# Optimization experiments

Measured on AMD Instinct MI355X. Metric: run time of the kernel, lower is better.

## Reference

```python
import jax, jax.numpy as jnp
import numpy as np

BS = 64; T = 96; C = 16; IN = 16; H = 256; NH = 8; DH = H // NH
NCLS = 4; L = T + NCLS; LAYERS = 4; GDEP = 2; EPS = 1e-5


def _ln(x, g, b):
    m = x.mean(-1, keepdims=True)
    v = ((x - m) ** 2).mean(-1, keepdims=True)
    return (x - m) / jnp.sqrt(v + EPS) * g + b


def _mask():
    # causal upper-triangular -inf mask; last NCLS rows (cls tokens) attend everywhere
    m = jnp.where(jnp.triu(jnp.ones((L, L), jnp.float32), 1) > 0, -jnp.inf, 0.0)
    return m.at[-NCLS:].set(0.0)


def _enc(h, mask, Wqkv, bqkv, Wo, bo, W1, b1, W2, b2, g1, be1, g2, be2):
    # post-norm TransformerEncoderLayer (torch default), dropout=0
    B = h.shape[0]
    qkv = h @ Wqkv.T + bqkv
    q, k, v = jnp.split(qkv, 3, axis=-1)
    sp = lambda t: t.reshape(B, L, NH, DH).transpose(0, 2, 1, 3)
    q, k, v = sp(q), sp(k), sp(v)
    s = jnp.einsum('bhqd,bhkd->bhqk', q, k) / np.float32(np.sqrt(DH)) + mask
    a = jax.nn.softmax(s, axis=-1)
    o = jnp.einsum('bhqk,bhkd->bhqd', a, v).transpose(0, 2, 1, 3).reshape(B, L, H)
    h = _ln(h + o @ Wo.T + bo, g1, be1)
    ff = jax.nn.relu(h @ W1.T + b1) @ W2.T + b2
    return _ln(h + ff, g2, be2)


def _mixprop(x, g, Wm, bm):
    # x: (bs, H, C, NCLS); MTGNN mixprop with alpha=0
    adj = g + jnp.eye(C, dtype=g.dtype)
    a = adj / adj.sum(1, keepdims=True)
    h = x
    outs = [x]
    for _ in range(GDEP):
        h = jnp.einsum('ncwl,vw->ncvl', h, a)
        outs.append(h)
    ho = jnp.concatenate(outs, axis=1)  # (bs, (GDEP+1)*H, C, NCLS)
    return jnp.einsum('ncwl,oc->nowl', ho, Wm) + bm[None, :, None, None]


def _forward(x, Wfc, bfc, cls_token, pos_emb, emb1, emb2, Wl1, bl1, Wl2, bl2,
             Wqkv, bqkv, Wo, bo, W1, b1, W2, b2, ln1g, ln1b, ln2g, ln2b,
             Wmlp, bmlp, Wd1, bd1, Wd2, bd2):
    bs = x.shape[0]
    h = x @ Wfc.T + bfc                                      # (bs,T,C,H)
    h = jnp.concatenate([h, jnp.broadcast_to(cls_token, (bs, NCLS, C, H))], axis=1)
    h = h + pos_emb[None]                                    # (bs,L,C,H)
    h = jnp.swapaxes(h, 1, 2).reshape(bs * C, L, H)
    mask = _mask()
    # graph_constructor (alpha=1)
    m1 = jnp.tanh(emb1 @ Wl1.T + bl1)
    m2 = jnp.tanh(emb2 @ Wl2.T + bl2)
    g = jax.nn.relu(jnp.tanh(m1 @ m2.T - m2 @ m1.T))         # (C,C)
    h = _enc(h, mask, Wqkv[0], bqkv[0], Wo[0], bo[0], W1[0], b1[0], W2[0], b2[0],
             ln1g[0], ln1b[0], ln2g[0], ln2b[0])
    for l in range(1, LAYERS):
        cls = h[:, -NCLS:].reshape(bs, C, NCLS, H).transpose(0, 3, 1, 2)  # (bs,H,C,NCLS)
        cls = _mixprop(cls, g, Wmlp[l - 1], bmlp[l - 1])
        cls = cls.transpose(0, 2, 3, 1).reshape(bs * C, NCLS, H)
        h = jnp.concatenate([h[:, :-NCLS], cls], axis=1)
        h = _enc(h, mask, Wqkv[l], bqkv[l], Wo[l], bo[l], W1[l], b1[l], W2[l], b2[l],
                 ln1g[l], ln1b[l], ln2g[l], ln2b[l])
    z = jnp.tanh(h[:, -NCLS:].reshape(bs, C * NCLS * H))
    z = jax.nn.gelu(z @ Wd1.T + bd1, approximate=False) @ Wd2.T + bd2
    return z[:, 0]


def setup_inputs() -> dict:
    key = jax.random.key(0)
    ks = iter(jax.random.split(key, 64))
    rn = lambda *s: jax.random.normal(next(ks), s, dtype=jnp.float32) * 0.05
    d = {}
    d['x'] = jax.random.normal(next(ks), (BS, T, C, IN), dtype=jnp.float32)
    d['p'] = jnp.zeros((BS,), jnp.float32)
    d['y'] = jnp.zeros((BS,), jnp.float32)
    d['Wfc'] = rn(H, IN); d['bfc'] = jnp.zeros((H,), jnp.float32)
    d['cls_token'] = rn(1, NCLS, C, H) * 20.0  # torch randn scale ~1
    d['pos_emb'] = rn(NCLS + T, C, H) * 20.0
    d['emb1'] = rn(C, H); d['emb2'] = rn(C, H)
    d['Wl1'] = rn(H, H); d['bl1'] = jnp.zeros((H,), jnp.float32)
    d['Wl2'] = rn(H, H); d['bl2'] = jnp.zeros((H,), jnp.float32)
    d['Wqkv'] = rn(LAYERS, 3 * H, H); d['bqkv'] = jnp.zeros((LAYERS, 3 * H), jnp.float32)
    d['Wo'] = rn(LAYERS, H, H); d['bo'] = jnp.zeros((LAYERS, H), jnp.float32)
    d['W1'] = rn(LAYERS, 4 * H, H); d['b1'] = jnp.zeros((LAYERS, 4 * H), jnp.float32)
    d['W2'] = rn(LAYERS, H, 4 * H); d['b2'] = jnp.zeros((LAYERS, H), jnp.float32)
    d['ln1g'] = jnp.ones((LAYERS, H), jnp.float32); d['ln1b'] = jnp.zeros((LAYERS, H), jnp.float32)
    d['ln2g'] = jnp.ones((LAYERS, H), jnp.float32); d['ln2b'] = jnp.zeros((LAYERS, H), jnp.float32)
    d['Wmlp'] = rn(LAYERS - 1, H, (GDEP + 1) * H); d['bmlp'] = jnp.zeros((LAYERS - 1, H), jnp.float32)
    d['Wd1'] = rn(H, NCLS * C * H); d['bd1'] = jnp.zeros((H,), jnp.float32)
    d['Wd2'] = rn(1, H); d['bd2'] = jnp.zeros((1,), jnp.float32)
    return d


def reference(x, p, y, Wfc, bfc, cls_token, pos_emb, emb1, emb2, Wl1, bl1, Wl2, bl2,
              Wqkv, bqkv, Wo, bo, W1, b1, W2, b2, ln1g, ln1b, ln2g, ln2b,
              Wmlp, bmlp, Wd1, bd1, Wd2, bd2):
    # p, y are unused by the original forward (kept for signature parity)
    return _forward(x, Wfc, bfc, cls_token, pos_emb, emb1, emb2, Wl1, bl1, Wl2, bl2,
                    Wqkv, bqkv, Wo, bo, W1, b1, W2, b2, ln1g, ln1b, ln2g, ln2b,
                    Wmlp, bmlp, Wd1, bd1, Wd2, bd2)
```

## Files before the change

kernel.cpp:

```cpp
#include <hip/hip_runtime.h>
#include <hip/hip_bf16.h>
#include <math.h>

typedef unsigned short u16;
typedef unsigned int   u32;
typedef __attribute__((ext_vector_type(8))) short short8;
typedef __attribute__((ext_vector_type(4))) float f32x4;

#define BSZ   64
#define TT    96
#define CCH   16
#define INDIM 16
#define HD    256
#define NHEAD 8
#define DHEAD 32
#define NCLS  4
#define LSEQ  100
#define NLAY  4
#define EPSV  1e-5f
#define BSEQ  (BSZ*CCH)
#define MTOK  (BSEQ*LSEQ)

#if __has_builtin(__builtin_amdgcn_exp2f)
#define EXP2F __builtin_amdgcn_exp2f
#else
#define EXP2F exp2f
#endif

__device__ __forceinline__ float bf2f(u16 x){ return __uint_as_float(((u32)x)<<16); }
__device__ __forceinline__ u16 f2bf(float f){
    u32 u = __float_as_uint(f);
    u32 r = (u + 0x7fffu + ((u>>16)&1u)) >> 16;
    return (u16)r;
}
__device__ __forceinline__ float lo16(u32 r){ return __uint_as_float(r<<16); }
__device__ __forceinline__ float hi16(u32 r){ return __uint_as_float(r&0xffff0000u); }

__device__ __forceinline__ u32 cvtpk(float lo, float hi){
    u32 r;
    asm("v_cvt_pk_bf16_f32 %0, %1, %2" : "=v"(r) : "v"(lo), "v"(hi));
    return r;
}

__device__ __forceinline__ void gload_lds16(const u16* g, u16* l){
    __builtin_amdgcn_global_load_lds(
        (const __attribute__((address_space(1))) unsigned int*)g,
        (__attribute__((address_space(3))) unsigned int*)l, 16, 0, 0);
}

__global__ __launch_bounds__(256)
void k_cvt(const float* __restrict__ src, u16* __restrict__ dst, int n)
{
    for (int i = blockIdx.x*256 + threadIdx.x; i < n; i += gridDim.x*256)
        dst[i] = f2bf(src[i]);
}

__global__ __launch_bounds__(256)
void k_embed(const float* __restrict__ x, const float* __restrict__ Wfc,
             const float* __restrict__ bfc, const float* __restrict__ cls,
             const float* __restrict__ pos, u16* __restrict__ h)
{
    int s = blockIdx.x;
    int n = s >> 4, c = s & 15;
    int hc = threadIdx.x;
    float wr[INDIM];
    #pragma unroll
    for (int i=0;i<INDIM;i++) wr[i] = Wfc[hc*INDIM + i];
    float bb = bfc[hc];
    for (int l=0; l<TT; l++){
        const float* xr = x + (size_t)((n*TT + l)*CCH + c)*INDIM;
        float acc = bb;
        #pragma unroll
        for (int i=0;i<INDIM;i++) acc += xr[i]*wr[i];
        acc += pos[(size_t)(l*CCH + c)*HD + hc];
        h[((size_t)s*LSEQ + l)*HD + hc] = f2bf(acc);
    }
    #pragma unroll
    for (int l=TT; l<LSEQ; l++){
        float v = cls[(size_t)((l-TT)*CCH + c)*HD + hc]
                + pos[(size_t)(l*CCH + c)*HD + hc];
        h[((size_t)s*LSEQ + l)*HD + hc] = f2bf(v);
    }
}

__global__ __launch_bounds__(256)
void k_graph_m(const float* __restrict__ emb, const float* __restrict__ Wl,
               const float* __restrict__ bl, float* __restrict__ m)
{
    int r = blockIdx.x, o = threadIdx.x;
    __shared__ float e[HD];
    e[o] = emb[r*HD + o];
    __syncthreads();
    const float* w = Wl + (size_t)o*HD;
    float acc = bl[o];
    for (int k=0;k<HD;k++) acc += e[k]*w[k];
    m[r*HD + o] = tanhf(acc);
}

__global__ __launch_bounds__(256)
void k_graph_a(const float* __restrict__ m1, const float* __restrict__ m2,
               float* __restrict__ a)
{
    int t = threadIdx.x; int v = t >> 4, w = t & 15;
    __shared__ float adj[16][17];
    float s1=0.f, s2=0.f;
    for (int k=0;k<HD;k++){
        s1 += m1[v*HD+k]*m2[w*HD+k];
        s2 += m2[v*HD+k]*m1[w*HD+k];
    }
    float g = tanhf(s1 - s2); g = g > 0.f ? g : 0.f;
    adj[v][w] = g + (v==w ? 1.f : 0.f);
    __syncthreads();
    float rs = 0.f;
    #pragma unroll
    for (int j=0;j<16;j++) rs += adj[v][j];
    a[t] = adj[v][w] / rs;
}

__global__ __launch_bounds__(256)
void k_gemmA(const u16* __restrict__ A, int lda,
             const u16* __restrict__ W, const float* __restrict__ bias,
             u16* __restrict__ C, int ldc, int K, int relu, int scat)
{
    __shared__ u16 smem[32768];
    u16* As0 = smem;
    u16* As1 = smem + 8192;
    u16* Ws0 = smem + 16384;
    u16* Ws1 = smem + 24576;

    int t = threadIdx.x;
    int lane = t & 63, w = t >> 6;
    int wm = (w & 1)*64, wn = (w >> 1)*64;
    int fr = lane & 15, quad = lane >> 4;

    int nwg = gridDim.x * gridDim.y;
    int bid = blockIdx.y * gridDim.x + blockIdx.x;
    int tile = bid;
    if (!(nwg & 7)){
        int cpx = nwg >> 3;
        tile = (bid & 7)*cpx + (bid >> 3);
    }
    int bx = tile % gridDim.x, by = tile / gridDim.x;
    size_t mb = (size_t)by * 128;
    int nb = bx * 128;

    int srow = lane >> 2;
    int sslot = lane & 3;

    f32x4 acc[4][4] = {};

    auto STAGE = [&](int bb, int k0){
        #pragma unroll
        for (int i=0;i<2;i++){
            int r = w*32 + i*16 + srow;
            int cw = sslot ^ ((r>>1)&3);
            gload_lds16(&A[(mb + r)*(size_t)lda + k0      + cw*8], &As0[bb*4096 + (w*32 + i*16)*32]);
            gload_lds16(&A[(mb + r)*(size_t)lda + k0 + 32 + cw*8], &As1[bb*4096 + (w*32 + i*16)*32]);
            gload_lds16(&W[(size_t)(nb + r)*K   + k0      + cw*8], &Ws0[bb*4096 + (w*32 + i*16)*32]);
            gload_lds16(&W[(size_t)(nb + r)*K   + k0 + 32 + cw*8], &Ws1[bb*4096 + (w*32 + i*16)*32]);
        }
    };
    auto COMPUTE = [&](int bb){
        short8 af0[4], af1[4], bf0[4], bf1[4];
        #pragma unroll
        for (int mt=0; mt<4; mt++){
            int r = wm + mt*16 + fr;
            int sw = (quad ^ ((r>>1)&3)) << 3;
            af0[mt] = *(const short8*)&As0[bb*4096 + r*32 + sw];
            af1[mt] = *(const short8*)&As1[bb*4096 + r*32 + sw];
        }
        #pragma unroll
        for (int nt=0; nt<4; nt++){
            int r = wn + nt*16 + fr;
            int sw = (quad ^ ((r>>1)&3)) << 3;
            bf0[nt] = *(const short8*)&Ws0[bb*4096 + r*32 + sw];
            bf1[nt] = *(const short8*)&Ws1[bb*4096 + r*32 + sw];
        }
        #pragma unroll
        for (int mt=0; mt<4; mt++)
            #pragma unroll
            for (int nt=0; nt<4; nt++){
                acc[mt][nt] = __builtin_amdgcn_mfma_f32_16x16x32_bf16(
                    af0[mt], bf0[nt], acc[mt][nt], 0, 0, 0);
                acc[mt][nt] = __builtin_amdgcn_mfma_f32_16x16x32_bf16(
                    af1[mt], bf1[nt], acc[mt][nt], 0, 0, 0);
            }
    };

    const int nst = K >> 6;
    STAGE(0, 0);
    asm volatile("s_waitcnt vmcnt(0)" ::: "memory");
    __builtin_amdgcn_s_barrier();
    int b = 0;
    for (int ts = 0; ts < nst; ++ts){
        if (ts + 1 < nst) STAGE(b^1, (ts+1) << 6);
        COMPUTE(b);
        asm volatile("s_waitcnt vmcnt(0)" ::: "memory");
        __builtin_amdgcn_s_barrier();
        b ^= 1;
    }

    float bb4[4];
    #pragma unroll
    for (int nt=0; nt<4; nt++) bb4[nt] = bias[nb + wn + nt*16 + fr];
    __syncthreads();
    u16* Ct = smem;
    #pragma unroll
    for (int mt=0; mt<4; mt++){
        int rw = wm + mt*16 + quad*4;
        #pragma unroll
        for (int nt=0; nt<4; nt++){
            int col = wn + nt*16 + fr;
            float v0 = acc[mt][nt][0] + bb4[nt];
            float v1 = acc[mt][nt][1] + bb4[nt];
            float v2 = acc[mt][nt][2] + bb4[nt];
            float v3 = acc[mt][nt][3] + bb4[nt];
            if (relu){
                v0 = v0 > 0.f ? v0 : 0.f;  v1 = v1 > 0.f ? v1 : 0.f;
                v2 = v2 > 0.f ? v2 : 0.f;  v3 = v3 > 0.f ? v3 : 0.f;
            }
            u32 p01 = cvtpk(v0, v1), p23 = cvtpk(v2, v3);
            Ct[(rw+0)*128 + col] = (u16)p01;
            Ct[(rw+1)*128 + col] = (u16)(p01 >> 16);
            Ct[(rw+2)*128 + col] = (u16)p23;
            Ct[(rw+3)*128 + col] = (u16)(p23 >> 16);
        }
    }
    __syncthreads();
    #pragma unroll
    for (int it=0; it<8; ++it){
        int row = it*16 + (t>>4);
        int seg = t & 15;
        size_t rg = mb + row;
        if (scat) rg = (rg >> 2)*LSEQ + TT + (rg & 3);
        *(short8*)&C[rg*(size_t)ldc + nb + seg*8] = *(const short8*)&Ct[row*128 + seg*8];
    }
}

__global__ __launch_bounds__(256)
void k_gemmC(const u16* __restrict__ A, int lda, int K,
             const u16* __restrict__ W, const float* __restrict__ bias,
             u16* __restrict__ h, const float* __restrict__ gam,
             const float* __restrict__ bet, size_t row0)
{
    __shared__ u16 smem[40960];
    u16* As0 = smem;
    u16* As1 = smem + 4096;
    u16* Ws0 = smem + 8192;
    u16* Ws1 = smem + 24576;

    int t = threadIdx.x;
    int lane = t & 63, w = t >> 6;
    int fr = lane & 15, quad = lane >> 4;
    size_t mb = (size_t)blockIdx.x * 64;
    int srow = lane >> 2, sslot = lane & 3;

    f32x4 acc[4][4] = {};

    auto STAGE = [&](int bb, int k0){
        {
            int r = w*16 + srow;
            int cw = sslot ^ ((r>>1)&3);
            gload_lds16(&A[(mb + r)*(size_t)lda + k0      + cw*8], &As0[bb*2048 + (w*16)*32]);
            gload_lds16(&A[(mb + r)*(size_t)lda + k0 + 32 + cw*8], &As1[bb*2048 + (w*16)*32]);
        }
        #pragma unroll
        for (int i=0;i<4;i++){
            int r = w*64 + i*16 + srow;
            int cw = sslot ^ ((r>>1)&3);
            gload_lds16(&W[(size_t)r*K + k0      + cw*8], &Ws0[bb*8192 + (w*64 + i*16)*32]);
            gload_lds16(&W[(size_t)r*K + k0 + 32 + cw*8], &Ws1[bb*8192 + (w*64 + i*16)*32]);
        }
    };
    auto COMPUTE = [&](int bb){
        short8 af0[4], af1[4], bf0[4], bf1[4];
        #pragma unroll
        for (int mt=0; mt<4; mt++){
            int ra = mt*16 + fr;
            int swa = (quad ^ ((ra>>1)&3)) << 3;
            af0[mt] = *(const short8*)&As0[bb*2048 + ra*32 + swa];
            af1[mt] = *(const short8*)&As1[bb*2048 + ra*32 + swa];
        }
        #pragma unroll
        for (int nt=0; nt<4; nt++){
            int rb = w*64 + nt*16 + fr;
            int swb = (quad ^ ((rb>>1)&3)) << 3;
            bf0[nt] = *(const short8*)&Ws0[bb*8192 + rb*32 + swb];
            bf1[nt] = *(const short8*)&Ws1[bb*8192 + rb*32 + swb];
        }
        #pragma unroll
        for (int mt=0; mt<4; mt++)
            #pragma unroll
            for (int nt=0; nt<4; nt++){
                acc[mt][nt] = __builtin_amdgcn_mfma_f32_16x16x32_bf16(
                    af0[mt], bf0[nt], acc[mt][nt], 0, 0, 0);
                acc[mt][nt] = __builtin_amdgcn_mfma_f32_16x16x32_bf16(
                    af1[mt], bf1[nt], acc[mt][nt], 0, 0, 0);
            }
    };

    const int nst = K >> 6;
    STAGE(0, 0);
    asm volatile("s_waitcnt vmcnt(0)" ::: "memory");
    __builtin_amdgcn_s_barrier();
    int b = 0;
    for (int ts = 0; ts < nst; ++ts){
        if (ts + 1 < nst) STAGE(b^1, (ts+1) << 6);
        COMPUTE(b);
        asm volatile("s_waitcnt vmcnt(0)" ::: "memory");
        __builtin_amdgcn_s_barrier();
        b ^= 1;
    }

    float bb4[4], gg[4], be[4];
    #pragma unroll
    for (int nt=0; nt<4; nt++){
        int col = w*64 + nt*16 + fr;
        bb4[nt] = bias[col]; gg[nt] = gam[col]; be[nt] = bet[col];
    }
    #pragma unroll
    for (int mt=0; mt<4; mt++){
        #pragma unroll
        for (int r=0; r<4; r++){
            size_t row = row0 + mb + mt*16 + quad*4 + r;
            #pragma unroll
            for (int nt=0; nt<4; nt++)
                acc[mt][nt][r] += bb4[nt] + bf2f(h[row*HD + w*64 + nt*16 + fr]);
        }
    }
    __syncthreads();
    float* red  = (float*)smem;
    float* red2 = (float*)(smem + 512);
    float ps[4][4];
    #pragma unroll
    for (int mt=0; mt<4; mt++)
        #pragma unroll
        for (int r=0; r<4; r++){
            float s = acc[mt][0][r] + acc[mt][1][r] + acc[mt][2][r] + acc[mt][3][r];
            s += __shfl_xor(s,1,64); s += __shfl_xor(s,2,64);
            s += __shfl_xor(s,4,64); s += __shfl_xor(s,8,64);
            ps[mt][r] = s;
        }
    if (fr == 0){
        #pragma unroll
        for (int mt=0; mt<4; mt++)
            #pragma unroll
            for (int r=0; r<4; r++)
                red[w*64 + mt*16 + quad*4 + r] = ps[mt][r];
    }
    __syncthreads();
    float mean[4][4];
    #pragma unroll
    for (int mt=0; mt<4; mt++)
        #pragma unroll
        for (int r=0; r<4; r++){
            int rl = mt*16 + quad*4 + r;
            mean[mt][r] = (red[rl] + red[64+rl] + red[128+rl] + red[192+rl]) * (1.f/256.f);
            float s = 0.f;
            #pragma unroll
            for (int nt=0; nt<4; nt++){ float d = acc[mt][nt][r] - mean[mt][r]; s += d*d; }
            s += __shfl_xor(s,1,64); s += __shfl_xor(s,2,64);
            s += __shfl_xor(s,4,64); s += __shfl_xor(s,8,64);
            ps[mt][r] = s;
        }
    if (fr == 0){
        #pragma unroll
        for (int mt=0; mt<4; mt++)
            #pragma unroll
            for (int r=0; r<4; r++)
                red2[w*64 + mt*16 + quad*4 + r] = ps[mt][r];
    }
    __syncthreads();
    u16* Ct = smem + 8192;
    #pragma unroll
    for (int mt=0; mt<4; mt++)
        #pragma unroll
        for (int r=0; r<4; r++){
            int rl = mt*16 + quad*4 + r;
            float inv = rsqrtf((red2[rl] + red2[64+rl] + red2[128+rl] + red2[192+rl])
                               * (1.f/256.f) + EPSV);
            float o0 = (acc[mt][0][r] - mean[mt][r]) * inv * gg[0] + be[0];
            float o1 = (acc[mt][1][r] - mean[mt][r]) * inv * gg[1] + be[1];
            float o2 = (acc[mt][2][r] - mean[mt][r]) * inv * gg[2] + be[2];
            float o3 = (acc[mt][3][r] - mean[mt][r]) * inv * gg[3] + be[3];
            u32 p01 = cvtpk(o0, o1), p23 = cvtpk(o2, o3);
            Ct[rl*256 + w*64 +  0 + fr] = (u16)p01;
            Ct[rl*256 + w*64 + 16 + fr] = (u16)(p01 >> 16);
            Ct[rl*256 + w*64 + 32 + fr] = (u16)p23;
            Ct[rl*256 + w*64 + 48 + fr] = (u16)(p23 >> 16);
        }
    __syncthreads();
    #pragma unroll
    for (int it=0; it<8; ++it){
        int row = it*8 + (t>>5);
        int seg = t & 31;
        *(short8*)&h[(row0 + mb + row)*HD + seg*8] = *(const short8*)&Ct[row*256 + seg*8];
    }
}

#define KS_STR 40
#define VT_STR 136
__global__ __launch_bounds__(256)
void k_attn(u16* __restrict__ qkv)
{
    __shared__ u16 smem[17664];
    int t = threadIdx.x;
    int w = t >> 6, lane = t & 63;
    int fr = lane & 15, quad = lane >> 4;
    int p = t >> 7, t2 = t & 127;
    u16* Ks = smem + p*4480;
    u16* Vt = smem + 8960 + p*4352;

    {
        int gp = blockIdx.x*2 + p;
        size_t base = (size_t)(gp >> 3)*LSEQ*768 + (gp & 7)*32;
        for (int idx = t2; idx < 1792; idx += 128){
            int key = idx >> 4, d2 = (idx & 15) << 1;
            u32 kv = (key < LSEQ) ? *(const u32*)&qkv[base + (size_t)key*768 + 256 + d2] : 0u;
            *(u32*)&Ks[key*KS_STR + d2] = kv;
        }
        for (int idx = t2; idx < 2048; idx += 128){
            int key = idx & 127, d2 = (idx >> 7) << 1;
            u32 vv = (key < LSEQ) ? *(const u32*)&qkv[base + (size_t)key*768 + 512 + d2] : 0u;
            Vt[ d2   *VT_STR + key] = (u16)(vv & 0xffffu);
            Vt[(d2+1)*VT_STR + key] = (u16)(vv >> 16);
        }
    }
    __syncthreads();

    int wp = w >> 1;
    int gp = blockIdx.x*2 + wp;
    size_t base = (size_t)(gp >> 3)*LSEQ*768 + (gp & 7)*32;
    u16* Ksw = smem + wp*4480;
    u16* Vtw = smem + 8960 + wp*4352;

    short8 kf[7];
    #pragma unroll
    for (int nt=0; nt<7; nt++)
        kf[nt] = *(const short8*)&Ksw[(nt*16 + fr)*KS_STR + quad*8];
    short8 vfr[4][2];
    #pragma unroll
    for (int ks=0; ks<4; ks++)
        #pragma unroll
        for (int nt=0; nt<2; nt++)
            vfr[ks][nt] = *(const short8*)&Vtw[(nt*16 + fr)*VT_STR + ks*32 + quad*8];

    const int smask = (w & 1) ? 0x34 : 0x4B;
    short8 qfs[7];
    #pragma unroll
    for (int st=0; st<7; ++st){
        if (!((smask >> st) & 1)) continue;
        int q = st*16 + fr;
        short8 z = {};
        qfs[st] = (q < LSEQ) ? *(const short8*)&qkv[base + (size_t)q*768 + quad*8] : z;
    }
    __syncthreads();

    u16* Ph = smem + w*2048;
    u16* Pv = smem + 8960 + w*2048;

    const float cs = 0.17677669529663687f * 1.4426950408889634f;
    #pragma unroll
    for (int st = 0; st < 7; ++st){
        if (!((smask >> st) & 1)) continue;
        const int ntile = (st == 6) ? 7 : (st + 1);
        const int nks   = (st == 6) ? 4 : (st/2 + 1);
        f32x4 S[7];
        #pragma unroll
        for (int nt=0; nt<7; nt++){
            if (nt >= ntile) continue;
            f32x4 z = {};
            S[nt] = __builtin_amdgcn_mfma_f32_16x16x32_bf16(qfs[st], kf[nt], z, 0,0,0);
        }
        float mx[4] = {-1e30f,-1e30f,-1e30f,-1e30f};
        #pragma unroll
        for (int nt=0;nt<7;nt++){
            if (nt >= ntile) continue;
            #pragma unroll
            for (int r=0;r<4;r++){
                float s = S[nt][r]*cs;
                if (nt == ntile-1){
                    int qr = st*16 + quad*4 + r;
                    int jmax = (qr < TT) ? qr : (LSEQ-1);
                    s = ((nt*16 + fr) <= jmax) ? s : -1e30f;
                }
                S[nt][r] = s;
                mx[r] = fmaxf(mx[r], s);
            }
        }
        #pragma unroll
        for (int r=0;r<4;r++){
            #pragma unroll
            for (int m=1;m<16;m<<=1) mx[r] = fmaxf(mx[r], __shfl_xor(mx[r], m, 64));
        }
        float l4[4] = {0.f,0.f,0.f,0.f};
        #pragma unroll
        for (int r=0;r<4;r++){
            #pragma unroll
            for (int nt=0;nt<7;nt++){
                if (nt >= ntile) continue;
                float pv = EXP2F(S[nt][r] - mx[r]);
                S[nt][r] = pv;
                l4[r] += pv;
            }
        }
        #pragma unroll
        for (int r=0;r<4;r++){
            #pragma unroll
            for (int m=1;m<16;m<<=1) l4[r] += __shfl_xor(l4[r], m, 64);
        }
        asm volatile("s_waitcnt lgkmcnt(0)" ::: "memory");
        #pragma unroll
        for (int nt=0;nt<7;nt++){
            if (nt >= ntile) continue;
            u32 h01 = cvtpk(S[nt][0], S[nt][1]);
            u32 h23 = cvtpk(S[nt][2], S[nt][3]);
            float l0 = S[nt][0] - lo16(h01);
            float l1 = S[nt][1] - hi16(h01);
            float l2 = S[nt][2] - lo16(h23);
            float l3 = S[nt][3] - hi16(h23);
            u32 g01 = cvtpk(l0, l1);
            u32 g23 = cvtpk(l2, l3);
            u16 hv[4] = {(u16)h01, (u16)(h01>>16), (u16)h23, (u16)(h23>>16)};
            u16 lv[4] = {(u16)g01, (u16)(g01>>16), (u16)g23, (u16)(g23>>16)};
            #pragma unroll
            for (int r=0;r<4;r++){
                int row = quad*4 + r;
                int a = (nt>>1)*512 + row*32 + ((((nt&1)<<4) + fr) ^ (((row>>1)&3)<<3));
                Ph[a] = hv[r];
                Pv[a] = lv[r];
            }
        }
        if (ntile*16 < nks*32){
            #pragma unroll
            for (int r=0;r<4;r++){
                int row = quad*4 + r;
                int a = (ntile>>1)*512 + row*32 + ((((ntile&1)<<4) + fr) ^ (((row>>1)&3)<<3));
                Ph[a] = 0;
                Pv[a] = 0;
            }
        }
        asm volatile("s_waitcnt lgkmcnt(0)" ::: "memory");
        f32x4 D[2] = {};
        #pragma unroll
        for (int ks=0; ks<4; ks++){
            if (ks >= nks) continue;
            int a = ks*512 + fr*32 + ((quad ^ ((fr>>1)&3)) << 3);
            short8 ph = *(const short8*)&Ph[a];
            short8 pl = *(const short8*)&Pv[a];
            #pragma unroll
            for (int nt=0; nt<2; nt++){
                D[nt] = __builtin_amdgcn_mfma_f32_16x16x32_bf16(ph, vfr[ks][nt], D[nt], 0,0,0);
                D[nt] = __builtin_amdgcn_mfma_f32_16x16x32_bf16(pl, vfr[ks][nt], D[nt], 0,0,0);
            }
        }
        #pragma unroll
        for (int r=0;r<4;r++){
            int qr = st*16 + quad*4 + r;
            if (qr < LSEQ){
                float inv = 1.f / l4[r];
                u32 o = cvtpk(D[0][r]*inv, D[1][r]*inv);
                qkv[base + (size_t)qr*768 +      fr] = (u16)o;
                qkv[base + (size_t)qr*768 + 16 + fr] = (u16)(o >> 16);
            }
        }
    }
}

__global__ __launch_bounds__(256)
void k_mixprep(const u16* __restrict__ h, const float* __restrict__ a,
               u16* __restrict__ amid)
{
    int n = blockIdx.x >> 2, tt = blockIdx.x & 3;
    __shared__ float xs[256][17], h1s[256][17], h2s[256][17];
    __shared__ float as[16][17];
    int t = threadIdx.x;
    as[t>>4][t&15] = a[t];
    for (int idx=t; idx<4096; idx+=256){
        int w = idx >> 8, hc = idx & 255;
        xs[hc][w] = bf2f(h[((size_t)(n*16 + w)*LSEQ + TT + tt)*HD + hc]);
    }
    __syncthreads();
    for (int idx=t; idx<4096; idx+=256){
        int v = idx & 15, hc = idx >> 4;
        float acc = 0.f;
        #pragma unroll
        for (int w=0;w<16;w++) acc += as[v][w]*xs[hc][w];
        h1s[hc][v] = acc;
    }
    __syncthreads();
    for (int idx=t; idx<4096; idx+=256){
        int v = idx & 15, hc = idx >> 4;
        float acc = 0.f;
        #pragma unroll
        for (int w=0;w<16;w++) acc += as[v][w]*h1s[hc][w];
        h2s[hc][v] = acc;
    }
    __syncthreads();
    int hc = t;
    #pragma unroll
    for (int w=0;w<16;w++){
        size_t row = (size_t)((n*16 + w)*4 + tt);
        amid[row*768 +       hc] = f2bf(xs[hc][w]);
        amid[row*768 + 256 + hc] = f2bf(h1s[hc][w]);
        amid[row*768 + 512 + hc] = f2bf(h2s[hc][w]);
    }
}

__global__ __launch_bounds__(256)
void k_z(const u16* __restrict__ h, u16* __restrict__ z)
{
    int bid = blockIdx.x, t = threadIdx.x;
    #pragma unroll
    for (int tc=0;tc<4;tc++)
        z[((size_t)bid*4 + tc)*HD + t] = f2bf(tanhf(bf2f(h[((size_t)bid*LSEQ + TT + tc)*HD + t])));
}

__global__ __launch_bounds__(256)
void k_head1p(const u16* __restrict__ z, const float* __restrict__ Wd1,
              float* __restrict__ d1p)
{
    __shared__ float zch[64][137];
    __shared__ float wt[16][137];
    int t = threadIdx.x;
    int col = t & 15, rgrp = t >> 4;
    int ob = blockIdx.x * 16;
    int kb = blockIdx.y;
    float acc[4] = {0.f,0.f,0.f,0.f};
    for (int kc=0; kc<1024; kc+=128){
        int base_k = kb*1024 + kc;
        #pragma unroll
        for (int jj=0; jj<16; jj++){
            int idx = t + jj*256;
            int n = idx >> 6, k2 = (idx & 63) << 1;
            u32 r = *(const u32*)&z[(size_t)n*16384 + base_k + k2];
            zch[n][k2] = lo16(r); zch[n][k2+1] = hi16(r);
        }
        #pragma unroll
        for (int jj=0; jj<2; jj++){
            int idx = t + jj*256;
            int r = idx >> 5, k4 = (idx & 31) << 2;
            float4 w4 = *(const float4*)&Wd1[(size_t)(ob + r)*16384 + base_k + k4];
            wt[r][k4] = w4.x; wt[r][k4+1] = w4.y; wt[r][k4+2] = w4.z; wt[r][k4+3] = w4.w;
        }
        __syncthreads();
        for (int k=0;k<128;k++){
            float wv = wt[col][k];
            #pragma unroll
            for (int u=0;u<4;u++) acc[u] += zch[rgrp + 16*u][k]*wv;
        }
        __syncthreads();
    }
    #pragma unroll
    for (int u=0;u<4;u++)
        d1p[(size_t)(kb*64 + rgrp + 16*u)*HD + ob + col] = acc[u];
}

__global__ __launch_bounds__(256)
void k_headf(const float* __restrict__ d1p, const float* __restrict__ bd1,
             const float* __restrict__ Wd2, const float* __restrict__ bd2,
             float* __restrict__ out)
{
    __shared__ float red[4];
    int n = blockIdx.x, c = threadIdx.x;
    float s = 0.f;
    #pragma unroll
    for (int kb=0; kb<16; kb++) s += d1p[(size_t)(kb*64 + n)*HD + c];
    float xx = s + bd1[c];
    float ge = 0.5f*xx*(1.f + erff(xx*0.70710678118654752f));
    float p = ge * Wd2[c];
    #pragma unroll
    for (int m=1;m<64;m<<=1) p += __shfl_xor(p, m, 64);
    if ((c & 63) == 0) red[c >> 6] = p;
    __syncthreads();
    if (c == 0) out[n] = red[0]+red[1]+red[2]+red[3] + bd2[0];
}

extern "C" void kernel_launch(void* const* d_in, const int* in_sizes, int n_in,
                              void* d_out, int out_size, void* d_ws, size_t ws_size,
                              hipStream_t stream)
{
    const float* x    = (const float*)d_in[0];
    const float* Wfc  = (const float*)d_in[3];
    const float* bfc  = (const float*)d_in[4];
    const float* cls  = (const float*)d_in[5];
    const float* pos  = (const float*)d_in[6];
    const float* emb1 = (const float*)d_in[7];
    const float* emb2 = (const float*)d_in[8];
    const float* Wl1  = (const float*)d_in[9];
    const float* bl1  = (const float*)d_in[10];
    const float* Wl2  = (const float*)d_in[11];
    const float* bl2  = (const float*)d_in[12];
    const float* Wqkv = (const float*)d_in[13];
    const float* bqkv = (const float*)d_in[14];
    const float* Wo   = (const float*)d_in[15];
    const float* bo   = (const float*)d_in[16];
    const float* W1   = (const float*)d_in[17];
    const float* b1   = (const float*)d_in[18];
    const float* W2   = (const float*)d_in[19];
    const float* b2   = (const float*)d_in[20];
    const float* ln1g = (const float*)d_in[21];
    const float* ln1b = (const float*)d_in[22];
    const float* ln2g = (const float*)d_in[23];
    const float* ln2b = (const float*)d_in[24];
    const float* Wmlp = (const float*)d_in[25];
    const float* bmlp = (const float*)d_in[26];
    const float* Wd1  = (const float*)d_in[27];
    const float* bd1  = (const float*)d_in[28];
    const float* Wd2  = (const float*)d_in[29];
    const float* bd2  = (const float*)d_in[30];

    int NCH = 8;
    {
        const size_t fixed = 63145088 + (1<<20);
        if      (fixed + (size_t)MTOK    *2048 <= ws_size) NCH = 1;
        else if (fixed + (size_t)(MTOK/2)*2048 <= ws_size) NCH = 2;
        else if (fixed + (size_t)(MTOK/4)*2048 <= ws_size) NCH = 4;
    }
    const int RCH = MTOK / NCH;
    const int SCH = BSEQ / NCH;

    u16* h    = (u16*)d_ws;
    u16* buf  = h    + (size_t)MTOK*HD;
    u16* wq   = buf  + (size_t)RCH*1024;
    u16* wo   = wq   + (size_t)4*768*256;
    u16* w1   = wo   + (size_t)4*256*256;
    u16* w2   = w1   + (size_t)4*1024*256;
    u16* wmb  = w2   + (size_t)4*256*1024;
    u16* zb   = wmb  + (size_t)3*256*768;
    float* fp = (float*)(zb + (size_t)BSZ*16384);
    float* m1  = fp;
    float* m2  = m1 + CCH*HD;
    float* an  = m2 + CCH*HD;
    float* d1p = an + CCH*CCH;

    k_cvt<<<512, 256, 0, stream>>>(Wqkv, wq, 4*768*256);
    k_cvt<<<256, 256, 0, stream>>>(Wo,   wo, 4*256*256);
    k_cvt<<<512, 256, 0, stream>>>(W1,   w1, 4*1024*256);
    k_cvt<<<512, 256, 0, stream>>>(W2,   w2, 4*256*1024);
    k_cvt<<<256, 256, 0, stream>>>(Wmlp, wmb, 3*256*768);

    k_embed<<<BSEQ, 256, 0, stream>>>(x, Wfc, bfc, cls, pos, h);
    k_graph_m<<<16, 256, 0, stream>>>(emb1, Wl1, bl1, m1);
    k_graph_m<<<16, 256, 0, stream>>>(emb2, Wl2, bl2, m2);
    k_graph_a<<<1, 256, 0, stream>>>(m1, m2, an);

    for (int l=0; l<NLAY; l++){
        if (l > 0){
            k_mixprep<<<BSZ*NCLS, 256, 0, stream>>>(h, an, buf);
            k_gemmA<<<dim3(256/128, 4096/128), 256, 0, stream>>>(
                buf, 768, wmb + (size_t)(l-1)*256*768, bmlp + (size_t)(l-1)*HD,
                h, HD, 768, 0, 1);
        }

        for (int c=0; c<NCH; c++){
            size_t row0 = (size_t)c * RCH;
            k_gemmA<<<dim3(768/128, RCH/128), 256, 0, stream>>>(
                h + row0*HD, HD, wq + (size_t)l*768*256, bqkv + (size_t)l*768,
                buf, 768, HD, 0, 0);
            k_attn<<<SCH*NHEAD/2, 256, 0, stream>>>(buf);
            k_gemmC<<<RCH/64, 256, 0, stream>>>(
                buf, 768, HD, wo + (size_t)l*256*256, bo + (size_t)l*HD,
                h, ln1g + (size_t)l*HD, ln1b + (size_t)l*HD, row0);
            k_gemmA<<<dim3(1024/128, RCH/128), 256, 0, stream>>>(
                h + row0*HD, HD, w1 + (size_t)l*1024*256, b1 + (size_t)l*1024,
                buf, 1024, HD, 1, 0);
            k_gemmC<<<RCH/64, 256, 0, stream>>>(
                buf, 1024, 1024, w2 + (size_t)l*256*1024, b2 + (size_t)l*HD,
                h, ln2g + (size_t)l*HD, ln2b + (size_t)l*HD, row0);
        }
    }

    k_z<<<BSZ*CCH, 256, 0, stream>>>(h, zb);
    k_head1p<<<dim3(16, 16), 256, 0, stream>>>(zb, Wd1, d1p);
    k_headf<<<BSZ, 256, 0, stream>>>(d1p, bd1, Wd2, bd2, (float*)d_out);
}
```

Before: 2.041 ms.

## Load GEMM fragments directly from global into registers, bypassing LDS staging

Both GEMM kernels (gemmA and gemmC) drop the LDS double-buffer filled by global_load_lds. Each wave now loads its MFMA operand fragments straight from global memory into a register double buffer, and the barriers are removed. This cuts LDS traffic, the barriers, and shared-memory footprint, which may raise occupancy. In exchange, waves no longer share tiles, so global and L2 reads are duplicated across waves, and register pressure rises.

```diff
diff --git a/kernel.cpp b/kernel.cpp
--- a/kernel.cpp
+++ b/kernel.cpp
@@ -42,12 +42,6 @@
     return r;
 }
 
-__device__ __forceinline__ void gload_lds16(const u16* g, u16* l){
-    __builtin_amdgcn_global_load_lds(
-        (const __attribute__((address_space(1))) unsigned int*)g,
-        (__attribute__((address_space(3))) unsigned int*)l, 16, 0, 0);
-}
-
 __global__ __launch_bounds__(256)
 void k_cvt(const float* __restrict__ src, u16* __restrict__ dst, int n)
 {
@@ -122,12 +116,7 @@
              const u16* __restrict__ W, const float* __restrict__ bias,
              u16* __restrict__ C, int ldc, int K, int relu, int scat)
 {
-    __shared__ u16 smem[32768];
-    u16* As0 = smem;
-    u16* As1 = smem + 8192;
-    u16* Ws0 = smem + 16384;
-    u16* Ws1 = smem + 24576;
-
+    __shared__ u16 smem[16384];
     int t = threadIdx.x;
     int lane = t & 63, w = t >> 6;
     int wm = (w & 1)*64, wn = (w >> 1)*64;
@@ -144,66 +133,51 @@
     size_t mb = (size_t)by * 128;
     int nb = bx * 128;
 
-    int srow = lane >> 2;
-    int sslot = lane & 3;
+    const u16* Ab[4]; const u16* Wb[4];
+    #pragma unroll
+    for (int i=0;i<4;i++){
+        Ab[i] = A + (mb + wm + i*16 + fr)*(size_t)lda + quad*8;
+        Wb[i] = W + (size_t)(nb + wn + i*16 + fr)*K + quad*8;
+    }
 
     f32x4 acc[4][4] = {};
-
-    auto STAGE = [&](int bb, int k0){
-        #pragma unroll
-        for (int i=0;i<2;i++){
-            int r = w*32 + i*16 + srow;
-            int cw = sslot ^ ((r>>1)&3);
-            gload_lds16(&A[(mb + r)*(size_t)lda + k0      + cw*8], &As0[bb*4096 + (w*32 + i*16)*32]);
-            gload_lds16(&A[(mb + r)*(size_t)lda + k0 + 32 + cw*8], &As1[bb*4096 + (w*32 + i*16)*32]);
-            gload_lds16(&W[(size_t)(nb + r)*K   + k0      + cw*8], &Ws0[bb*4096 + (w*32 + i*16)*32]);
-            gload_lds16(&W[(size_t)(nb + r)*K   + k0 + 32 + cw*8], &Ws1[bb*4096 + (w*32 + i*16)*32]);
-        }
-    };
-    auto COMPUTE = [&](int bb){
-        short8 af0[4], af1[4], bf0[4], bf1[4];
-        #pragma unroll
-        for (int mt=0; mt<4; mt++){
-            int r = wm + mt*16 + fr;
-            int sw = (quad ^ ((r>>1)&3)) << 3;
-            af0[mt] = *(const short8*)&As0[bb*4096 + r*32 + sw];
-            af1[mt] = *(const short8*)&As1[bb*4096 + r*32 + sw];
-        }
-        #pragma unroll
-        for (int nt=0; nt<4; nt++){
-            int r = wn + nt*16 + fr;
-            int sw = (quad ^ ((r>>1)&3)) << 3;
-            bf0[nt] = *(const short8*)&Ws0[bb*4096 + r*32 + sw];
-            bf1[nt] = *(const short8*)&Ws1[bb*4096 + r*32 + sw];
-        }
-        #pragma unroll
-        for (int mt=0; mt<4; mt++)
-            #pragma unroll
-            for (int nt=0; nt<4; nt++){
-                acc[mt][nt] = __builtin_amdgcn_mfma_f32_16x16x32_bf16(
-                    af0[mt], bf0[nt], acc[mt][nt], 0, 0, 0);
-                acc[mt][nt] = __builtin_amdgcn_mfma_f32_16x16x32_bf16(
-                    af1[mt], bf1[nt], acc[mt][nt], 0, 0, 0);
-            }
-    };
+    short8 fa0[2][4], fa1[2][4], fb0[2][4], fb1[2][4];
+
+#define GLOADA(S, k0) { \
+    _Pragma("unroll") \
+    for (int i=0;i<4;i++){ \
+        fa0[S][i] = *(const short8*)(Ab[i] + (k0)); \
+        fa1[S][i] = *(const short8*)(Ab[i] + (k0) + 32); \
+        fb0[S][i] = *(const short8*)(Wb[i] + (k0)); \
+        fb1[S][i] = *(const short8*)(Wb[i] + (k0) + 32); \
+    } }
+
+#define GMFMAA(S) { \
+    _Pragma("unroll") \
+    for (int mt=0; mt<4; mt++) \
+        _Pragma("unroll") \
+        for (int nt=0; nt<4; nt++){ \
+            acc[mt][nt] = __builtin_amdgcn_mfma_f32_16x16x32_bf16(fa0[S][mt], fb0[S][nt], acc[mt][nt], 0,0,0); \
+            acc[mt][nt] = __builtin_amdgcn_mfma_f32_16x16x32_bf16(fa1[S][mt], fb1[S][nt], acc[mt][nt], 0,0,0); \
+        } }
 
     const int nst = K >> 6;
-    STAGE(0, 0);
-    asm volatile("s_waitcnt vmcnt(0)" ::: "memory");
-    __builtin_amdgcn_s_barrier();
-    int b = 0;
-    for (int ts = 0; ts < nst; ++ts){
-        if (ts + 1 < nst) STAGE(b^1, (ts+1) << 6);
-        COMPUTE(b);
-        asm volatile("s_waitcnt vmcnt(0)" ::: "memory");
-        __builtin_amdgcn_s_barrier();
-        b ^= 1;
-    }
+    GLOADA(0, 0)
+    int ts = 0;
+    for (;;){
+        if (ts + 1 < nst) GLOADA(1, (ts+1) << 6)
+        GMFMAA(0)
+        if (++ts == nst) break;
+        if (ts + 1 < nst) GLOADA(0, (ts+1) << 6)
+        GMFMAA(1)
+        if (++ts == nst) break;
+    }
+#undef GLOADA
+#undef GMFMAA
 
     float bb4[4];
     #pragma unroll
     for (int nt=0; nt<4; nt++) bb4[nt] = bias[nb + wn + nt*16 + fr];
-    __syncthreads();
     u16* Ct = smem;
     #pragma unroll
     for (int mt=0; mt<4; mt++){
@@ -243,74 +217,53 @@
              u16* __restrict__ h, const float* __restrict__ gam,
              const float* __restrict__ bet, size_t row0)
 {
-    __shared__ u16 smem[40960];
-    u16* As0 = smem;
-    u16* As1 = smem + 4096;
-    u16* Ws0 = smem + 8192;
-    u16* Ws1 = smem + 24576;
-
+    __shared__ u16 smem[17408];
     int t = threadIdx.x;
     int lane = t & 63, w = t >> 6;
     int fr = lane & 15, quad = lane >> 4;
     size_t mb = (size_t)blockIdx.x * 64;
-    int srow = lane >> 2, sslot = lane & 3;
+
+    const u16* Ab[4]; const u16* Wb[4];
+    #pragma unroll
+    for (int i=0;i<4;i++){
+        Ab[i] = A + (mb + i*16 + fr)*(size_t)lda + quad*8;
+        Wb[i] = W + (size_t)(w*64 + i*16 + fr)*K + quad*8;
+    }
 
     f32x4 acc[4][4] = {};
-
-    auto STAGE = [&](int bb, int k0){
-        {
-            int r = w*16 + srow;
-            int cw = sslot ^ ((r>>1)&3);
-            gload_lds16(&A[(mb + r)*(size_t)lda + k0      + cw*8], &As0[bb*2048 + (w*16)*32]);
-            gload_lds16(&A[(mb + r)*(size_t)lda + k0 + 32 + cw*8], &As1[bb*2048 + (w*16)*32]);
-        }
-        #pragma unroll
-        for (int i=0;i<4;i++){
-            int r = w*64 + i*16 + srow;
-            int cw = sslot ^ ((r>>1)&3);
-            gload_lds16(&W[(size_t)r*K + k0      + cw*8], &Ws0[bb*8192 + (w*64 + i*16)*32]);
-            gload_lds16(&W[(size_t)r*K + k0 + 32 + cw*8], &Ws1[bb*8192 + (w*64 + i*16)*32]);
-        }
-    };
-    auto COMPUTE = [&](int bb){
-        short8 af0[4], af1[4], bf0[4], bf1[4];
-        #pragma unroll
-        for (int mt=0; mt<4; mt++){
-            int ra = mt*16 + fr;
-            int swa = (quad ^ ((ra>>1)&3)) << 3;
-            af0[mt] = *(const short8*)&As0[bb*2048 + ra*32 + swa];
-            af1[mt] = *(const short8*)&As1[bb*2048 + ra*32 + swa];
-        }
-        #pragma unroll
-        for (int nt=0; nt<4; nt++){
-            int rb = w*64 + nt*16 + fr;
-            int swb = (quad ^ ((rb>>1)&3)) << 3;
-            bf0[nt] = *(const short8*)&Ws0[bb*8192 + rb*32 + swb];
-            bf1[nt] = *(const short8*)&Ws1[bb*8192 + rb*32 + swb];
-        }
-        #pragma unroll
-        for (int mt=0; mt<4; mt++)
-            #pragma unroll
-            for (int nt=0; nt<4; nt++){
-                acc[mt][nt] = __builtin_amdgcn_mfma_f32_16x16x32_bf16(
-                    af0[mt], bf0[nt], acc[mt][nt], 0, 0, 0);
-                acc[mt][nt] = __builtin_amdgcn_mfma_f32_16x16x32_bf16(
-                    af1[mt], bf1[nt], acc[mt][nt], 0, 0, 0);
-            }
-    };
+    short8 fa0[2][4], fa1[2][4], fb0[2][4], fb1[2][4];
+
+#define GLOADC(S, k0) { \
+    _Pragma("unroll") \
+    for (int i=0;i<4;i++){ \
+        fa0[S][i] = *(const short8*)(Ab[i] + (k0)); \
+        fa1[S][i] = *(const short8*)(Ab[i] + (k0) + 32); \
+        fb0[S][i] = *(const short8*)(Wb[i] + (k0)); \
+        fb1[S][i] = *(const short8*)(Wb[i] + (k0) + 32); \
+    } }
+
+#define GMFMAC(S) { \
+    _Pragma("unroll") \
+    for (int mt=0; mt<4; mt++) \
+        _Pragma("unroll") \
+        for (int nt=0; nt<4; nt++){ \
+            acc[mt][nt] = __builtin_amdgcn_mfma_f32_16x16x32_bf16(fa0[S][mt], fb0[S][nt], acc[mt][nt], 0,0,0); \
+            acc[mt][nt] = __builtin_amdgcn_mfma_f32_16x16x32_bf16(fa1[S][mt], fb1[S][nt], acc[mt][nt], 0,0,0); \
+        } }
 
     const int nst = K >> 6;
-    STAGE(0, 0);
-    asm volatile("s_waitcnt vmcnt(0)" ::: "memory");
-    __builtin_amdgcn_s_barrier();
-    int b = 0;
-    for (int ts = 0; ts < nst; ++ts){
-        if (ts + 1 < nst) STAGE(b^1, (ts+1) << 6);
-        COMPUTE(b);
-        asm volatile("s_waitcnt vmcnt(0)" ::: "memory");
-        __builtin_amdgcn_s_barrier();
-        b ^= 1;
-    }
+    GLOADC(0, 0)
+    int ts = 0;
+    for (;;){
+        if (ts + 1 < nst) GLOADC(1, (ts+1) << 6)
+        GMFMAC(0)
+        if (++ts == nst) break;
+        if (ts + 1 < nst) GLOADC(0, (ts+1) << 6)
+        GMFMAC(1)
+        if (++ts == nst) break;
+    }
+#undef GLOADC
+#undef GMFMAC
 
     float bb4[4], gg[4], be[4];
     #pragma unroll
@@ -328,7 +281,6 @@
                 acc[mt][nt][r] += bb4[nt] + bf2f(h[row*HD + w*64 + nt*16 + fr]);
         }
     }
-    __syncthreads();
     float* red  = (float*)smem;
     float* red2 = (float*)(smem + 512);
     float ps[4][4];
@@ -371,7 +323,7 @@
                 red2[w*64 + mt*16 + quad*4 + r] = ps[mt][r];
     }
     __syncthreads();
-    u16* Ct = smem + 8192;
+    u16* Ct = smem + 1024;
     #pragma unroll
     for (int mt=0; mt<4; mt++)
         #pragma unroll
```

Measured after the change: 4.084 ms. +100.1%, slower.
